# Kernel tuning notes

Hardware: AMD Instinct MI355X
Metric: run time of the kernel (lower is better)

## Reference

```python
import jax, jax.numpy as jnp
import numpy as np
import math

LMAX = 2
NUM_Z = 4
N_NODES = 20000
N_GRAPHS = 5000
N_EDGES = 320000
# irreps as (mul, l, parity)
IR_SH   = [(1, 0, 1), (1, 1, -1), (1, 2, 1)]
IR_ATTR = [(NUM_Z**2, 0, 1), (NUM_Z**2, 1, -1), (NUM_Z**2, 2, 1)]
IR_MID  = [(64, 0, 1), (24, 1, 1), (24, 1, -1), (16, 2, 1), (16, 2, -1)]
IR_OUT  = [(1, 0, -1), (6, 0, 1)]


def _cg(j1, j2, j3, m1, m2, m3):
    if m1 + m2 != m3:
        return 0.0
    f = math.factorial
    pre = math.sqrt((2 * j3 + 1) * f(j3 + j1 - j2) * f(j3 - j1 + j2) * f(j1 + j2 - j3) / f(j1 + j2 + j3 + 1))
    pre *= math.sqrt(f(j3 + m3) * f(j3 - m3) * f(j1 - m1) * f(j1 + m1) * f(j2 - m2) * f(j2 + m2))
    s = 0.0
    for k in range(max(0, j2 - j3 - m1, j1 - j3 + m2), min(j1 + j2 - j3, j1 - m1, j2 + m2) + 1):
        s += (-1) ** k / (f(k) * f(j1 + j2 - j3 - k) * f(j1 - m1 - k) * f(j2 + m2 - k) * f(j3 - j2 + m1 + k) * f(j3 - j1 - m2 + k))
    return pre * s


def _u(l):
    # complex -> real spherical harmonics change of basis, m = -l..l
    U = np.zeros((2 * l + 1, 2 * l + 1), dtype=complex)
    for m in range(-l, l + 1):
        if m > 0:
            U[m + l, -m + l] = 1 / math.sqrt(2)
            U[m + l, m + l] = (-1) ** m / math.sqrt(2)
        elif m == 0:
            U[l, l] = 1.0
        else:
            U[m + l, m + l] = 1j / math.sqrt(2)
            U[m + l, -m + l] = -1j * (-1) ** (-m) / math.sqrt(2)
    return U


def _w3j(l1, l2, l3):
    C = np.zeros((2 * l1 + 1, 2 * l2 + 1, 2 * l3 + 1))
    for m1 in range(-l1, l1 + 1):
        for m2 in range(-l2, l2 + 1):
            m3 = m1 + m2
            if -l3 <= m3 <= l3:
                C[m1 + l1, m2 + l2, m3 + l3] = _cg(l1, l2, l3, m1, m2, m3)
    T = np.einsum('am,bn,co,mno->abc', _u(l1), _u(l2), _u(l3).conj(), C.astype(complex))
    T = T.real if np.abs(T.real).max() >= np.abs(T.imag).max() else T.imag
    return (T / np.linalg.norm(T)).astype(np.float32)  # Frobenius norm 1, e3nn convention


W3J = {(a, b, c): _w3j(a, b, c) for a in range(3) for b in range(3) for c in range(3) if abs(a - b) <= c <= a + b}


def _slices(ir):
    s = [0]
    for m, l, _ in ir:
        s.append(s[-1] + m * (2 * l + 1))
    return s


def _paths(ir1, ir2, iro):
    paths = []
    fan = [0] * len(iro)
    off = 0
    for a, (m1, l1, p1) in enumerate(ir1):
        for b, (m2, l2, p2) in enumerate(ir2):
            for c, (m3, l3, p3) in enumerate(iro):
                if p1 * p2 == p3 and abs(l1 - l2) <= l3 <= l1 + l2:
                    paths.append((a, b, c, off))
                    fan[c] += m1 * m2
                    off += m1 * m2 * m3
    return paths, fan, off


def _fctp(x1, x2, w, ir1, ir2, iro):
    # FullyConnectedTensorProduct: 'uvw' weighted Clebsch-Gordan contraction per path
    s1, s2 = _slices(ir1), _slices(ir2)
    paths, fan, _ = _paths(ir1, ir2, iro)
    E = x1.shape[0]
    out = [jnp.zeros((E, m * (2 * l + 1)), x1.dtype) for m, l, _ in iro]
    for a, b, c, off in paths:
        m1, l1, _ = ir1[a]
        m2, l2, _ = ir2[b]
        m3, l3, _ = iro[c]
        W = w[off:off + m1 * m2 * m3].reshape(m1, m2, m3)
        C = jnp.asarray(W3J[(l1, l2, l3)], x1.dtype)
        xa = x1[:, s1[a]:s1[a + 1]].reshape(E, m1, 2 * l1 + 1)
        xb = x2[:, s2[b]:s2[b + 1]].reshape(E, m2, 2 * l2 + 1)
        alpha = math.sqrt(2 * l3 + 1) / math.sqrt(fan[c])
        y = jnp.einsum('eui,evj,ijk,uvw->ewk', xa, xb, C, W)
        out[c] = out[c] + (alpha * y).reshape(E, -1)
    return jnp.concatenate(out, axis=1)


def _sh(v):
    # component-normalized harmonic polynomials for l=0,1,2 (normalize=False)
    x, y, z = v[:, 0], v[:, 1], v[:, 2]
    r2 = x * x + y * y + z * z
    s3, s15, s5 = math.sqrt(3.0), math.sqrt(15.0), math.sqrt(5.0)
    sh1 = s3 * jnp.stack([y, z, x], axis=1)
    sh2 = jnp.stack([s15 * x * y, s15 * y * z, 0.5 * s5 * (3 * z * z - r2), s15 * x * z, 0.5 * s15 * (x * x - y * y)], axis=1)
    return jnp.concatenate([jnp.ones_like(x)[:, None], sh1, sh2], axis=1)  # [E, 9]


def _forward(pos, w_tp1, w_tp2, z, batch, edge_src, edge_dst):
    E = edge_src.shape[0]
    ev = pos[edge_src] - pos[edge_dst]
    sh = _sh(ev)
    zz = NUM_Z * z[edge_src] + z[edge_dst]
    zzf = jax.nn.one_hot(zz, NUM_Z ** 2, dtype=sh.dtype) * NUM_Z  # [E, 16]
    # 'uvu' TensorProduct of (16x0e) with sh: outer product per l block
    blocks = [(0, 1), (1, 4), (4, 9)]
    edge_attr = jnp.concatenate([(zzf[:, :, None] * sh[:, None, a:b]).reshape(E, -1) for a, b in blocks], axis=1)
    inv_nn = 1.0 / math.sqrt(3.0)  # num_neighbors = 3
    node = jax.ops.segment_sum(sh, edge_dst, num_segments=N_NODES) * inv_nn
    ef = _fctp(node[edge_src], edge_attr, w_tp1, IR_SH, IR_ATTR, IR_MID)
    node = jax.ops.segment_sum(ef, edge_dst, num_segments=N_NODES) * inv_nn
    ef = _fctp(node[edge_src], edge_attr, w_tp2, IR_MID, IR_ATTR, IR_OUT)
    node = jax.ops.segment_sum(ef, edge_dst, num_segments=N_NODES) * inv_nn
    return jax.ops.segment_sum(node, batch, num_segments=N_GRAPHS) * 0.5  # num_nodes = 4


def setup_inputs() -> dict:
    key = jax.random.key(0)
    k = jax.random.split(key, 7)
    _, _, n1 = _paths(IR_SH, IR_ATTR, IR_MID)
    _, _, n2 = _paths(IR_MID, IR_ATTR, IR_OUT)
    return {
        'pos': jax.random.normal(k[0], (N_NODES, 3), jnp.float32),
        'z': jax.random.randint(k[1], (N_NODES,), 0, NUM_Z, jnp.int32),
        'batch': jnp.sort(jax.random.randint(k[2], (N_NODES,), 0, N_GRAPHS, jnp.int32)),
        'edge_src': jax.random.randint(k[3], (N_EDGES,), 0, N_NODES, jnp.int32),
        'edge_dst': jax.random.randint(k[4], (N_EDGES,), 0, N_NODES, jnp.int32),
        'w_tp1': jax.random.normal(k[5], (n1,), jnp.float32),
        'w_tp2': jax.random.normal(k[6], (n2,), jnp.float32),
    }


def reference(pos, z, batch, edge_src, edge_dst, w_tp1, w_tp2):
    return _forward(pos, w_tp1, w_tp2, z, batch, edge_src, edge_dst)
```

## Files before the change

### kernel.cpp

```cpp
#include <hip/hip_runtime.h>


#define N_EDGES   320000
#define NN_NODES  20000
#define NN_GRAPHS 5000

__device__ __forceinline__ void sh_from_vec(float x, float y, float z,
                                            float* B1, float* B2) {
    const float s3   = 1.7320508075688772f;
    const float s15  = 3.8729833462074170f;
    const float s5h  = 1.1180339887498949f;
    const float s15h = 1.9364916731037085f;
    B1[0] = s3 * y; B1[1] = s3 * z; B1[2] = s3 * x;
    float r2 = x * x + y * y + z * z;
    B2[0] = s15 * x * y;
    B2[1] = s15 * y * z;
    B2[2] = s5h * (3.f * z * z - r2);
    B2[3] = s15 * x * z;
    B2[4] = s15h * (x * x - y * y);
}

__global__ __launch_bounds__(256) void k_zero(const float* __restrict__ pos,
                                              const float* __restrict__ w2,
                                              int* __restrict__ counts,
                                              float* __restrict__ out,
                                              float4* __restrict__ pos4,
                                              float* __restrict__ w2p) {
    int tid = blockIdx.x * blockDim.x + threadIdx.x;
    int stride = gridDim.x * blockDim.x;
    for (int i = tid; i < NN_NODES; i += stride) counts[i] = 0;
    for (int i = tid; i < NN_GRAPHS * 7; i += stride) out[i] = 0.f;
    for (int i = tid; i < NN_NODES; i += stride) {
        float4 p;
        p.x = pos[3 * i]; p.y = pos[3 * i + 1]; p.z = pos[3 * i + 2]; p.w = 0.f;
        pos4[i] = p;
    }
    const float cT0f =  0.02830690f;
    const float cT1f = -0.02635231f;
    const float cT2f = -0.01634300f;
    const float cT3f =  0.01265893f;
    const float cT4f =  0.02041241f;
    for (int idx = tid; idx < 16 * 64 * 64; idx += stride) {
        int jj = idx & 63;
        int u  = (idx >> 6) & 63;
        int q  = idx >> 12;
        float v = 0.f;
        if (jj < 6) {
            v = cT0f * w2[(u * 16 + q) * 6 + jj];
        } else if (jj < 9) {
            if (u < 24) v = cT1f * w2[6144 + u * 16 + q];
        } else if (jj < 27) {
            int w = (jj - 9) % 6;
            if (u < 24) v = cT2f * w2[6528 + (u * 16 + q) * 6 + w];
        } else if (jj < 57) {
            int w = (jj - 27) % 6;
            if (u < 16) v = cT3f * w2[8832 + (u * 16 + q) * 6 + w];
        } else if (jj < 62) {
            if (u < 16) v = cT4f * w2[10368 + u * 16 + q];
        }
        w2p[idx] = v;
    }
}

__global__ __launch_bounds__(256) void k_hist(const int* __restrict__ edst,
                                              int* __restrict__ counts) {
    int e = blockIdx.x * blockDim.x + threadIdx.x;
    if (e < N_EDGES) atomicAdd(&counts[edst[e]], 1);
}

__global__ __launch_bounds__(1024) void k_scan(const int* __restrict__ counts,
                                               int* __restrict__ start,
                                               int* __restrict__ cursor) {
    __shared__ int wsum[16];
    __shared__ int carry;
    __shared__ int tot;
    int tid = threadIdx.x;
    int wave = tid >> 6;
    int lane = tid & 63;
    if (tid == 0) carry = 0;
    __syncthreads();
    for (int base = 0; base < NN_NODES; base += 1024) {
        int i = base + tid;
        int v = (i < NN_NODES) ? counts[i] : 0;
        int x = v;
#pragma unroll
        for (int off = 1; off < 64; off <<= 1) {
            int y = __shfl_up(x, off, 64);
            if (lane >= off) x += y;
        }
        if (lane == 63) wsum[wave] = x;
        __syncthreads();
        if (tid < 16) {
            int w = wsum[tid];
            int xx = w;
#pragma unroll
            for (int off = 1; off < 16; off <<= 1) {
                int y = __shfl_up(xx, off, 64);
                if (tid >= off) xx += y;
            }
            wsum[tid] = xx - w;
            if (tid == 15) tot = xx;
        }
        __syncthreads();
        int excl = carry + wsum[wave] + x - v;
        if (i < NN_NODES) {
            start[i] = excl;
            cursor[i] = excl;
        }
        __syncthreads();
        if (tid == 0) carry += tot;
        __syncthreads();
    }
    if (tid == 0) start[NN_NODES] = carry;
}

__global__ __launch_bounds__(256) void k_fill(const int* __restrict__ esrc,
                                              const int* __restrict__ edst,
                                              const int* __restrict__ zarr,
                                              int* __restrict__ cursor,
                                              int* __restrict__ csr) {
    int e = blockIdx.x * blockDim.x + threadIdx.x;
    if (e >= N_EDGES) return;
    int d = edst[e];
    int s = esrc[e];
    int q = 4 * zarr[s] + zarr[d];
    int p = atomicAdd(&cursor[d], 1);
    csr[p] = s | (q << 16) | ((d & 15) << 20);
}

__global__ __launch_bounds__(256) void k_nodesh(const float4* __restrict__ pos4,
                                                const int* __restrict__ start,
                                                const int* __restrict__ csr,
                                                float* __restrict__ node_sh) {
    __shared__ float ns[16][12];
    int t = threadIdx.x;
    if (t < 192) ns[t / 12][t % 12] = 0.f;
    __syncthreads();
    int nbase = blockIdx.x * 16;
    int e0 = start[nbase], e1 = start[nbase + 16];
    for (int idx = e0 + t; idx < e1; idx += 256) {
        int pk = csr[idx];
        int s = pk & 0xFFFF;
        int r = (pk >> 20) & 15;
        float4 pd = pos4[nbase + r];
        float4 ps = pos4[s];
        float x = ps.x - pd.x;
        float y = ps.y - pd.y;
        float z = ps.z - pd.z;
        float B1[3], B2[5];
        sh_from_vec(x, y, z, B1, B2);
        float* nr = &ns[r][0];
        atomicAdd(nr + 0, 1.f);
        atomicAdd(nr + 1, B1[0]); atomicAdd(nr + 2, B1[1]); atomicAdd(nr + 3, B1[2]);
        atomicAdd(nr + 4, B2[0]); atomicAdd(nr + 5, B2[1]); atomicAdd(nr + 6, B2[2]);
        atomicAdd(nr + 7, B2[3]); atomicAdd(nr + 8, B2[4]);
    }
    __syncthreads();
    if (t < 144) {
        int r = t / 9, c = t % 9;
        const float inv_nn = 0.57735026918962576f;
        node_sh[(size_t)(nbase + r) * 12 + c] = ns[r][c] * inv_nn;
    }
}

template<int RB>
__device__ __forceinline__ void phase2_pass(const float* __restrict__ Gl,
                                            float (* __restrict__ smid)[368],
                                            const float* __restrict__ w1,
                                            int zpack, int j) {
    const int zp = zpack >> (2 * RB);
    float acc[8] = {0.f, 0.f, 0.f, 0.f, 0.f, 0.f, 0.f, 0.f};
    if (j < 64) {
        int w = j;
        for (int q = 0; q < 16; q++) {
            float wa = w1[q * 64 + w];
            float wb = w1[2048 + q * 64 + w];
            float wc = w1[5248 + q * 64 + w];
            int zdq = q & 3;
            const float* Gq = Gl + (q >> 2) * 51;
#pragma unroll
            for (int r2 = 0; r2 < 8; r2++) {
                if (((zp >> (2 * r2)) & 3) == zdq) {
                    const float* gq = Gq + (RB + r2) * 204;
                    acc[r2] += gq[0] * wa + gq[12] * wb + gq[42] * wc;
                }
            }
        }
#pragma unroll
        for (int r2 = 0; r2 < 8; r2++)
            smid[RB + r2][j] = 0.33333333333333333f * acc[r2];
    } else if (j < 136) {
        int tt = j - 64, w = tt / 3, k = tt - 3 * w;
        for (int q = 0; q < 16; q++) {
            float wa = w1[3072 + q * 24 + w];
            float wb = w1[6272 + q * 24 + w];
            int zdq = q & 3;
            const float* Gq = Gl + (q >> 2) * 51;
#pragma unroll
            for (int r2 = 0; r2 < 8; r2++) {
                if (((zp >> (2 * r2)) & 3) == zdq) {
                    const float* gq = Gq + (RB + r2) * 204;
                    acc[r2] += gq[13 + k] * wa + gq[43 + k] * wb;
                }
            }
        }
#pragma unroll
        for (int r2 = 0; r2 < 8; r2++)
            smid[RB + r2][j] = 0.70710678118654752f * acc[r2];
    } else if (j < 208) {
        int tt = j - 136, w = tt / 3, k = tt - 3 * w;
        for (int q = 0; q < 16; q++) {
            float wa = w1[1024 + q * 24 + w];
            float wb = w1[1664 + q * 24 + w];
            float wc = w1[3712 + q * 24 + w];
            float wd = w1[4608 + q * 24 + w];
            int zdq = q & 3;
            const float* Gq = Gl + (q >> 2) * 51;
#pragma unroll
            for (int r2 = 0; r2 < 8; r2++) {
                if (((zp >> (2 * r2)) & 3) == zdq) {
                    const float* gq = Gq + (RB + r2) * 204;
                    acc[r2] += gq[1 + k] * wa + gq[9 + k] * wb +
                               gq[21 + k] * wc + gq[34 + k] * wd;
                }
            }
        }
#pragma unroll
        for (int r2 = 0; r2 < 8; r2++)
            smid[RB + r2][j] = 0.5f * acc[r2];
    } else if (j < 288) {
        int tt = j - 208, w = tt / 5, k = tt - 5 * w;
        for (int q = 0; q < 16; q++) {
            float wa = w1[1408 + q * 16 + w];
            float wb = w1[3456 + q * 16 + w];
            float wc = w1[4352 + q * 16 + w];
            float wd = w1[6656 + q * 16 + w];
            int zdq = q & 3;
            const float* Gq = Gl + (q >> 2) * 51;
#pragma unroll
            for (int r2 = 0; r2 < 8; r2++) {
                if (((zp >> (2 * r2)) & 3) == zdq) {
                    const float* gq = Gq + (RB + r2) * 204;
                    acc[r2] += gq[4 + k] * wa + gq[16 + k] * wb +
                               gq[29 + k] * wc + gq[46 + k] * wd;
                }
            }
        }
#pragma unroll
        for (int r2 = 0; r2 < 8; r2++)
            smid[RB + r2][j] = 0.64549722436790280f * acc[r2];
    } else if (j < 368) {
        int tt = j - 288, w = tt / 5, k = tt - 5 * w;
        for (int q = 0; q < 16; q++) {
            float wa = w1[4096 + q * 16 + w];
            float wb = w1[4992 + q * 16 + w];
            int zdq = q & 3;
            const float* Gq = Gl + (q >> 2) * 51;
#pragma unroll
            for (int r2 = 0; r2 < 8; r2++) {
                if (((zp >> (2 * r2)) & 3) == zdq) {
                    const float* gq = Gq + (RB + r2) * 204;
                    acc[r2] += gq[24 + k] * wa + gq[37 + k] * wb;
                }
            }
        }
#pragma unroll
        for (int r2 = 0; r2 < 8; r2++)
            smid[RB + r2][j] = 0.91287092917527690f * acc[r2];
    }
}

__global__ __launch_bounds__(512, 4) void k_mid(const float4* __restrict__ pos4,
                                                const float* __restrict__ node_sh,
                                                const int* __restrict__ start,
                                                const int* __restrict__ csr,
                                                const float* __restrict__ w1,
                                                const int* __restrict__ zarr,
                                                const float* __restrict__ w2p,
                                                float* __restrict__ tab) {
    __shared__ float Gl[16 * 204];
    __shared__ float smid[16][368];
    __shared__ int szl[16];
    __shared__ int zcnt[4];
    __shared__ int zlist[4][16];
    int t = threadIdx.x;
    int nbase = blockIdx.x * 16;
    for (int i = t; i < 16 * 204; i += 512) Gl[i] = 0.f;
    if (t < 16) szl[t] = zarr[nbase + t];
    else if (t < 20) zcnt[t - 16] = 0;
    __syncthreads();

    int e0 = start[nbase], e1 = start[nbase + 16];

    const float r3  = 0.57735026918962576f;
    const float r5  = 0.44721359549995794f;
    const float r6  = 0.40824829046386302f;
    const float r10 = 0.31622776601683794f;
    const float s30 = 0.18257418583505536f;
    const float rt3 = 1.7320508075688772f;
    const float c222 = 0.58554004376911990f;
    const float q6 = 0.40824829046386302f;
    const float h6 = 0.20412414523193151f;
    const float h2 = 0.35355339059327376f;
    const float r2c = 0.70710678118654752f;

    for (int idx = e0 + t; idx < e1; idx += 512) {
        int pk = csr[idx];
        int s = pk & 0xFFFF;
        int zs = (pk >> 18) & 3;
        int r = (pk >> 20) & 15;
        float4 pd = pos4[nbase + r];
        float4 ps = pos4[s];
        float x = ps.x - pd.x;
        float y = ps.y - pd.y;
        float z = ps.z - pd.z;
        float B1[3], B2[5];
        sh_from_vec(x, y, z, B1, B2);
        const float4 nv0 = *(const float4*)(node_sh + s * 12);
        const float4 nv1 = *(const float4*)(node_sh + s * 12 + 4);
        float a0 = nv0.x;
        float A1[3] = {nv0.y, nv0.z, nv0.w};
        float A2[5] = {nv1.x, nv1.y, nv1.z, nv1.w, node_sh[s * 12 + 8]};
        float* gr = Gl + r * 204 + zs * 51;

        atomicAdd(gr + 0, a0);
        atomicAdd(gr + 1, a0 * B1[0] * r3);
        atomicAdd(gr + 2, a0 * B1[1] * r3);
        atomicAdd(gr + 3, a0 * B1[2] * r3);
        atomicAdd(gr + 4, a0 * B2[0] * r5);
        atomicAdd(gr + 5, a0 * B2[1] * r5);
        atomicAdd(gr + 6, a0 * B2[2] * r5);
        atomicAdd(gr + 7, a0 * B2[3] * r5);
        atomicAdd(gr + 8, a0 * B2[4] * r5);
        atomicAdd(gr + 9,  A1[0] * r3);
        atomicAdd(gr + 10, A1[1] * r3);
        atomicAdd(gr + 11, A1[2] * r3);
        atomicAdd(gr + 12, -r3 * (A1[0] * B1[0] + A1[1] * B1[1] + A1[2] * B1[2]));
        atomicAdd(gr + 13, -r6 * (A1[1] * B1[2] - A1[2] * B1[1]));
        atomicAdd(gr + 14, -r6 * (A1[2] * B1[0] - A1[0] * B1[2]));
        atomicAdd(gr + 15, -r6 * (A1[0] * B1[1] - A1[1] * B1[0]));
        atomicAdd(gr + 16, r10 * (A1[0] * B1[2] + A1[2] * B1[0]));
        atomicAdd(gr + 17, r10 * (A1[0] * B1[1] + A1[1] * B1[0]));
        atomicAdd(gr + 18, s30 * (2.f * A1[1] * B1[1] - A1[0] * B1[0] - A1[2] * B1[2]));
        atomicAdd(gr + 19, r10 * (A1[1] * B1[2] + A1[2] * B1[1]));
        atomicAdd(gr + 20, r10 * (A1[2] * B1[2] - A1[0] * B1[0]));
        {
            float Byy = -B2[2] * q6 - B2[4] * r2c;
            float Bzz = 2.f * B2[2] * q6;
            float Bxx = -B2[2] * q6 + B2[4] * r2c;
            float Bxy = B2[0] * r2c;
            float Byz = B2[1] * r2c;
            float Bxz = B2[3] * r2c;
            atomicAdd(gr + 21, -r5 * (Byy * A1[0] + Byz * A1[1] + Bxy * A1[2]));
            atomicAdd(gr + 22, -r5 * (Byz * A1[0] + Bzz * A1[1] + Bxz * A1[2]));
            atomicAdd(gr + 23, -r5 * (Bxy * A1[0] + Bxz * A1[1] + Bxx * A1[2]));
        }
        atomicAdd(gr + 24, -s30 * (B2[1] * A1[0] - B2[3] * A1[2] + 2.f * B2[4] * A1[1]));
        atomicAdd(gr + 25, -s30 * (-B2[0] * A1[0] - rt3 * B2[2] * A1[2] + B2[3] * A1[1] - B2[4] * A1[2]));
        atomicAdd(gr + 26, -s30 * (rt3 * B2[1] * A1[2] - rt3 * B2[3] * A1[0]));
        atomicAdd(gr + 27, -s30 * (B2[0] * A1[2] - B2[1] * A1[1] + rt3 * B2[2] * A1[0] - B2[4] * A1[0]));
        atomicAdd(gr + 28, -s30 * (-2.f * B2[0] * A1[1] + B2[1] * A1[2] + B2[3] * A1[0]));
        atomicAdd(gr + 29, A2[0] * r5);
        atomicAdd(gr + 30, A2[1] * r5);
        atomicAdd(gr + 31, A2[2] * r5);
        atomicAdd(gr + 32, A2[3] * r5);
        atomicAdd(gr + 33, A2[4] * r5);
        {
            float Ayy = -A2[2] * q6 - A2[4] * r2c;
            float Azz = 2.f * A2[2] * q6;
            float Axx = -A2[2] * q6 + A2[4] * r2c;
            float Axy = A2[0] * r2c;
            float Ayz = A2[1] * r2c;
            float Axz = A2[3] * r2c;
            atomicAdd(gr + 34, -r5 * (Ayy * B1[0] + Ayz * B1[1] + Axy * B1[2]));
            atomicAdd(gr + 35, -r5 * (Ayz * B1[0] + Azz * B1[1] + Axz * B1[2]));
            atomicAdd(gr + 36, -r5 * (Axy * B1[0] + Axz * B1[1] + Axx * B1[2]));
        }
        atomicAdd(gr + 37, s30 * (A2[1] * B1[0] - A2[3] * B1[2] + 2.f * A2[4] * B1[1]));
        atomicAdd(gr + 38, s30 * (-A2[0] * B1[0] - rt3 * A2[2] * B1[2] + A2[3] * B1[1] - A2[4] * B1[2]));
        atomicAdd(gr + 39, s30 * (rt3 * A2[1] * B1[2] - rt3 * A2[3] * B1[0]));
        atomicAdd(gr + 40, s30 * (A2[0] * B1[2] - A2[1] * B1[1] + rt3 * A2[2] * B1[0] - A2[4] * B1[0]));
        atomicAdd(gr + 41, s30 * (-2.f * A2[0] * B1[1] + A2[1] * B1[2] + A2[3] * B1[0]));
        atomicAdd(gr + 42, r5 * (A2[0] * B2[0] + A2[1] * B2[1] + A2[2] * B2[2] +
                                 A2[3] * B2[3] + A2[4] * B2[4]));
        atomicAdd(gr + 43, s30 * (-A2[0] * B2[1] + A2[1] * B2[0] +
                                  rt3 * (A2[2] * B2[3] - A2[3] * B2[2]) +
                                  A2[3] * B2[4] - A2[4] * B2[3]));
        atomicAdd(gr + 44, s30 * (-2.f * A2[0] * B2[4] + 2.f * A2[4] * B2[0] -
                                  A2[1] * B2[3] + A2[3] * B2[1]));
        atomicAdd(gr + 45, s30 * (A2[0] * B2[3] - A2[3] * B2[0] +
                                  rt3 * (A2[1] * B2[2] - A2[2] * B2[1]) +
                                  A2[1] * B2[4] - A2[4] * B2[1]));
        atomicAdd(gr + 46, -c222 * (-q6 * (A2[0] * B2[2] + A2[2] * B2[0]) +
                                    h2 * (A2[1] * B2[3] + A2[3] * B2[1])));
        atomicAdd(gr + 47, -c222 * (h6 * (A2[1] * B2[2] + A2[2] * B2[1]) -
                                    h2 * (A2[1] * B2[4] + A2[4] * B2[1]) +
                                    h2 * (A2[0] * B2[3] + A2[3] * B2[0])));
        atomicAdd(gr + 48, -c222 * (q6 * (A2[2] * B2[2] - A2[0] * B2[0] - A2[4] * B2[4]) +
                                    h6 * (A2[1] * B2[1] + A2[3] * B2[3])));
        atomicAdd(gr + 49, -c222 * (h6 * (A2[3] * B2[2] + A2[2] * B2[3]) +
                                    h2 * (A2[3] * B2[4] + A2[4] * B2[3]) +
                                    h2 * (A2[0] * B2[1] + A2[1] * B2[0])));
        atomicAdd(gr + 50, -c222 * (-q6 * (A2[4] * B2[2] + A2[2] * B2[4]) +
                                    h2 * (A2[3] * B2[3] - A2[1] * B2[1])));
    }
    __syncthreads();

    int zpack = 0;
#pragma unroll
    for (int r2 = 0; r2 < 16; r2++)
        zpack |= __builtin_amdgcn_readfirstlane(szl[r2]) << (2 * r2);

    if (t < 16) {
        int zsv = (zpack >> (2 * t)) & 3;
        int p = atomicAdd(&zcnt[zsv], 1);
        zlist[zsv][p] = t;
    }

    phase2_pass<0>(Gl, smid, w1, zpack, t);
    phase2_pass<8>(Gl, smid, w1, zpack, t);
    __syncthreads();

    {
        int wave = t >> 6;
        int lane = t & 63;
        int mbase, mstride, ulim;
        if (lane < 6)       { mbase = 0;                mstride = 1; ulim = 64; }
        else if (lane < 9)  { mbase = 64 + (lane - 6);  mstride = 3; ulim = 24; }
        else if (lane < 27) { mbase = 136 + (lane - 9) / 6;  mstride = 3; ulim = 24; }
        else if (lane < 57) { mbase = 208 + (lane - 27) / 6; mstride = 5; ulim = 16; }
        else if (lane < 62) { mbase = 288 + (lane - 57);     mstride = 5; ulim = 16; }
        else                { mbase = 0;                mstride = 0; ulim = 1; }
        int ulim1 = ulim - 1;

        int c0 = zcnt[0], c1 = zcnt[1], c2 = zcnt[2], c3 = zcnt[3];
        int np0 = (c0 + 1) >> 1, np1 = (c1 + 1) >> 1;
        int np2 = (c2 + 1) >> 1, np3 = (c3 + 1) >> 1;
        int o1 = np0, o2 = o1 + np1, o3 = o2 + np2;
        int total = o3 + np3;

        for (int item = wave; item < total; item += 8) {
            int zsv, pi, cnt;
            if (item < o1)      { zsv = 0; pi = item;      cnt = c0; }
            else if (item < o2) { zsv = 1; pi = item - o1; cnt = c1; }
            else if (item < o3) { zsv = 2; pi = item - o2; cnt = c2; }
            else                { zsv = 3; pi = item - o3; cnt = c3; }
            int r0 = zlist[zsv][2 * pi];
            int i1 = 2 * pi + 1;
            int has2 = (i1 < cnt);
            int r1 = has2 ? zlist[zsv][i1] : r0;
            const float* mr0 = &smid[r0][0];
            const float* mr1 = &smid[r1][0];
            const float* wp = w2p + (size_t)(4 * zsv) * 4096 + lane;
            float a00 = 0.f, a01 = 0.f, a02 = 0.f, a03 = 0.f;
            float a10 = 0.f, a11 = 0.f, a12 = 0.f, a13 = 0.f;
#pragma unroll 4
            for (int u = 0; u < 64; u++) {
                int um = (u < ulim) ? u : ulim1;
                float w0 = wp[u * 64];
                float w1v = wp[4096 + u * 64];
                float w2v = wp[8192 + u * 64];
                float w3v = wp[12288 + u * 64];
                float m0 = mr0[mbase + mstride * um];
                float m1 = mr1[mbase + mstride * um];
                a00 += m0 * w0;  a01 += m0 * w1v;
                a02 += m0 * w2v; a03 += m0 * w3v;
                a10 += m1 * w0;  a11 += m1 * w1v;
                a12 += m1 * w2v; a13 += m1 * w3v;
            }
            size_t b0 = ((size_t)(nbase + r0) * 4) * 64 + lane;
            tab[b0] = a00; tab[b0 + 64] = a01;
            tab[b0 + 128] = a02; tab[b0 + 192] = a03;
            if (has2) {
                size_t b1 = ((size_t)(nbase + r1) * 4) * 64 + lane;
                tab[b1] = a10; tab[b1 + 64] = a11;
                tab[b1 + 128] = a12; tab[b1 + 192] = a13;
            }
        }
    }
}

__global__ __launch_bounds__(512, 8) void k_out(const float4* __restrict__ pos4,
                                                const int* __restrict__ zarr,
                                                const int* __restrict__ batch,
                                                const int* __restrict__ start,
                                                const int* __restrict__ csr,
                                                const float* __restrict__ tab,
                                                float* __restrict__ out) {
    int wave = threadIdx.x >> 6;
    int lane = threadIdx.x & 63;
    int n = blockIdx.x * 8 + wave;
    float4 pd = pos4[n];
    int zd = zarr[n];
    int s0 = start[n], s1 = start[n + 1];

    int fsel, oidx;
    if (lane < 6)       { fsel = 0;                  oidx = lane + 1; }
    else if (lane < 9)  { fsel = 1 + (lane - 6);     oidx = 0; }
    else if (lane < 27) { fsel = 1 + (lane - 9) / 6; oidx = (lane - 9) % 6 + 1; }
    else if (lane < 57) { fsel = 4 + (lane - 27) / 6; oidx = (lane - 27) % 6 + 1; }
    else if (lane < 62) { fsel = 4 + (lane - 57);    oidx = 0; }
    else                { fsel = -1;                 oidx = 7; }
    float f0 = (fsel == 0) ? 1.f : 0.f;
    float f1 = (fsel == 1) ? 1.f : 0.f;
    float f2 = (fsel == 2) ? 1.f : 0.f;
    float f3 = (fsel == 3) ? 1.f : 0.f;
    float f4 = (fsel == 4) ? 1.f : 0.f;
    float f5 = (fsel == 5) ? 1.f : 0.f;
    float f6 = (fsel == 6) ? 1.f : 0.f;
    float f7 = (fsel == 7) ? 1.f : 0.f;
    float f8 = (fsel == 8) ? 1.f : 0.f;

    float acc = 0.f;
    int idx = s0;
    for (; idx + 1 < s1; idx += 2) {
        int pkA = __builtin_amdgcn_readfirstlane(csr[idx]);
        int pkB = __builtin_amdgcn_readfirstlane(csr[idx + 1]);
        int sA = pkA & 0xFFFF;
        int sB = pkB & 0xFFFF;
        float TA = tab[((size_t)sA * 4 + zd) * 64 + lane];
        float TB = tab[((size_t)sB * 4 + zd) * 64 + lane];
        float4 psA = pos4[sA];
        float4 psB = pos4[sB];
        float xA = psA.x - pd.x, yA = psA.y - pd.y, zA = psA.z - pd.z;
        float xB = psB.x - pd.x, yB = psB.y - pd.y, zB = psB.z - pd.z;
        float B1A[3], B2A[5], B1B[3], B2B[5];
        sh_from_vec(xA, yA, zA, B1A, B2A);
        sh_from_vec(xB, yB, zB, B1B, B2B);
        float fA = f0 + f1 * B1A[0] + f2 * B1A[1] + f3 * B1A[2]
                 + f4 * B2A[0] + f5 * B2A[1] + f6 * B2A[2]
                 + f7 * B2A[3] + f8 * B2A[4];
        float fB = f0 + f1 * B1B[0] + f2 * B1B[1] + f3 * B1B[2]
                 + f4 * B2B[0] + f5 * B2B[1] + f6 * B2B[2]
                 + f7 * B2B[3] + f8 * B2B[4];
        acc += TA * fA + TB * fB;
    }
    if (idx < s1) {
        int pk = __builtin_amdgcn_readfirstlane(csr[idx]);
        int s = pk & 0xFFFF;
        float T = tab[((size_t)s * 4 + zd) * 64 + lane];
        float4 ps = pos4[s];
        float x = ps.x - pd.x, y = ps.y - pd.y, z = ps.z - pd.z;
        float B1[3], B2[5];
        sh_from_vec(x, y, z, B1, B2);
        float factor = f0 + f1 * B1[0] + f2 * B1[1] + f3 * B1[2]
                     + f4 * B2[0] + f5 * B2[1] + f6 * B2[2]
                     + f7 * B2[3] + f8 * B2[4];
        acc += T * factor;
    }

    float ov[7];
#pragma unroll
    for (int w = 0; w < 7; w++) ov[w] = (oidx == w) ? acc : 0.f;
#pragma unroll
    for (int off = 32; off > 0; off >>= 1)
#pragma unroll
        for (int w = 0; w < 7; w++) ov[w] += __shfl_down(ov[w], off, 64);
    if (lane == 0) {
        float* og = out + batch[n] * 7;
#pragma unroll
        for (int w = 0; w < 7; w++) atomicAdd(og + w, ov[w]);
    }
}

extern "C" void kernel_launch(void* const* d_in, const int* in_sizes, int n_in,
                              void* d_out, int out_size, void* d_ws, size_t ws_size,
                              hipStream_t stream) {
    const float* pos  = (const float*)d_in[0];
    const int*   z    = (const int*)d_in[1];
    const int*   bat  = (const int*)d_in[2];
    const int*   esrc = (const int*)d_in[3];
    const int*   edst = (const int*)d_in[4];
    const float* w1   = (const float*)d_in[5];
    const float* w2   = (const float*)d_in[6];
    float* out = (float*)d_out;

    int*   wsI = (int*)d_ws;
    float* wsF = (float*)d_ws;
    int* counts  = wsI + 0;
    int* start   = wsI + 32768;
    int* cursor  = wsI + 65536;
    int* csr     = wsI + 98304;
    float4* pos4   = (float4*)(wsF + 425984);
    float* node_sh = wsF + 524288;
    float* w2p     = wsF + 786432;
    float* tab     = wsF + 1048576;

    k_zero<<<128, 256, 0, stream>>>(pos, w2, counts, out, pos4, w2p);
    k_hist<<<(N_EDGES + 255) / 256, 256, 0, stream>>>(edst, counts);
    k_scan<<<1, 1024, 0, stream>>>(counts, start, cursor);
    k_fill<<<(N_EDGES + 255) / 256, 256, 0, stream>>>(esrc, edst, z, cursor, csr);
    k_nodesh<<<NN_NODES / 16, 256, 0, stream>>>(pos4, start, csr, node_sh);
    k_mid<<<NN_NODES / 16, 512, 0, stream>>>(pos4, node_sh, start, csr, w1, z, w2p, tab);
    k_out<<<NN_NODES / 8, 512, 0, stream>>>(pos4, z, bat, start, csr, tab, out);
}
```

Baseline: 354.3 us.

## Split mid-feature contraction into separate table kernel via global buffer

Moves the per-node second-stage contraction (mid features times w2p into the 4x64 table) out of k_mid into a new k_tab kernel, with mid features written to global memory and reused in place as the table (row stride 368). This frees k_mid's large shared smid array and z-grouping logic, which could raise occupancy, and gives the contraction its own launch with one wave per node. The cost is an extra global round trip of the mid features, one more kernel launch, and the loss of the old two-node sharing of weight loads within a z-group.

```diff
diff --git a/kernel.cpp b/kernel.cpp
--- a/kernel.cpp
+++ b/kernel.cpp
@@ -165,7 +165,8 @@
 
 template<int RB>
 __device__ __forceinline__ void phase2_pass(const float* __restrict__ Gl,
-                                            float (* __restrict__ smid)[368],
+                                            float* __restrict__ mid,
+                                            int nbase,
                                             const float* __restrict__ w1,
                                             int zpack, int j) {
     const int zp = zpack >> (2 * RB);
@@ -188,7 +189,7 @@
         }
 #pragma unroll
         for (int r2 = 0; r2 < 8; r2++)
-            smid[RB + r2][j] = 0.33333333333333333f * acc[r2];
+            mid[(size_t)(nbase + RB + r2) * 368 + j] = 0.33333333333333333f * acc[r2];
     } else if (j < 136) {
         int tt = j - 64, w = tt / 3, k = tt - 3 * w;
         for (int q = 0; q < 16; q++) {
@@ -206,7 +207,7 @@
         }
 #pragma unroll
         for (int r2 = 0; r2 < 8; r2++)
-            smid[RB + r2][j] = 0.70710678118654752f * acc[r2];
+            mid[(size_t)(nbase + RB + r2) * 368 + j] = 0.70710678118654752f * acc[r2];
     } else if (j < 208) {
         int tt = j - 136, w = tt / 3, k = tt - 3 * w;
         for (int q = 0; q < 16; q++) {
@@ -227,7 +228,7 @@
         }
 #pragma unroll
         for (int r2 = 0; r2 < 8; r2++)
-            smid[RB + r2][j] = 0.5f * acc[r2];
+            mid[(size_t)(nbase + RB + r2) * 368 + j] = 0.5f * acc[r2];
     } else if (j < 288) {
         int tt = j - 208, w = tt / 5, k = tt - 5 * w;
         for (int q = 0; q < 16; q++) {
@@ -248,7 +249,7 @@
         }
 #pragma unroll
         for (int r2 = 0; r2 < 8; r2++)
-            smid[RB + r2][j] = 0.64549722436790280f * acc[r2];
+            mid[(size_t)(nbase + RB + r2) * 368 + j] = 0.64549722436790280f * acc[r2];
     } else if (j < 368) {
         int tt = j - 288, w = tt / 5, k = tt - 5 * w;
         for (int q = 0; q < 16; q++) {
@@ -266,7 +267,7 @@
         }
 #pragma unroll
         for (int r2 = 0; r2 < 8; r2++)
-            smid[RB + r2][j] = 0.91287092917527690f * acc[r2];
+            mid[(size_t)(nbase + RB + r2) * 368 + j] = 0.91287092917527690f * acc[r2];
     }
 }
 
@@ -276,18 +277,13 @@
                                                 const int* __restrict__ csr,
                                                 const float* __restrict__ w1,
                                                 const int* __restrict__ zarr,
-                                                const float* __restrict__ w2p,
-                                                float* __restrict__ tab) {
+                                                float* __restrict__ mid) {
     __shared__ float Gl[16 * 204];
-    __shared__ float smid[16][368];
     __shared__ int szl[16];
-    __shared__ int zcnt[4];
-    __shared__ int zlist[4][16];
     int t = threadIdx.x;
     int nbase = blockIdx.x * 16;
     for (int i = t; i < 16 * 204; i += 512) Gl[i] = 0.f;
     if (t < 16) szl[t] = zarr[nbase + t];
-    else if (t < 20) zcnt[t - 16] = 0;
     __syncthreads();
 
     int e0 = start[nbase], e1 = start[nbase + 16];
@@ -411,73 +407,51 @@
     for (int r2 = 0; r2 < 16; r2++)
         zpack |= __builtin_amdgcn_readfirstlane(szl[r2]) << (2 * r2);
 
-    if (t < 16) {
-        int zsv = (zpack >> (2 * t)) & 3;
-        int p = atomicAdd(&zcnt[zsv], 1);
-        zlist[zsv][p] = t;
-    }
-
-    phase2_pass<0>(Gl, smid, w1, zpack, t);
-    phase2_pass<8>(Gl, smid, w1, zpack, t);
+    phase2_pass<0>(Gl, mid, nbase, w1, zpack, t);
+    phase2_pass<8>(Gl, mid, nbase, w1, zpack, t);
+}
+
+__global__ __launch_bounds__(256, 8) void k_tab(const int* __restrict__ zarr,
+                                                const float* __restrict__ w2p,
+                                                float* __restrict__ mid) {
+    __shared__ float srow[4][368];
+    int t = threadIdx.x;
+    int nbase = blockIdx.x * 4;
+    for (int i = t; i < 4 * 368; i += 256) {
+        int r = i / 368, c = i - r * 368;
+        srow[r][c] = mid[(size_t)(nbase + r) * 368 + c];
+    }
     __syncthreads();
 
-    {
-        int wave = t >> 6;
-        int lane = t & 63;
-        int mbase, mstride, ulim;
-        if (lane < 6)       { mbase = 0;                mstride = 1; ulim = 64; }
-        else if (lane < 9)  { mbase = 64 + (lane - 6);  mstride = 3; ulim = 24; }
-        else if (lane < 27) { mbase = 136 + (lane - 9) / 6;  mstride = 3; ulim = 24; }
-        else if (lane < 57) { mbase = 208 + (lane - 27) / 6; mstride = 5; ulim = 16; }
-        else if (lane < 62) { mbase = 288 + (lane - 57);     mstride = 5; ulim = 16; }
-        else                { mbase = 0;                mstride = 0; ulim = 1; }
-        int ulim1 = ulim - 1;
-
-        int c0 = zcnt[0], c1 = zcnt[1], c2 = zcnt[2], c3 = zcnt[3];
-        int np0 = (c0 + 1) >> 1, np1 = (c1 + 1) >> 1;
-        int np2 = (c2 + 1) >> 1, np3 = (c3 + 1) >> 1;
-        int o1 = np0, o2 = o1 + np1, o3 = o2 + np2;
-        int total = o3 + np3;
-
-        for (int item = wave; item < total; item += 8) {
-            int zsv, pi, cnt;
-            if (item < o1)      { zsv = 0; pi = item;      cnt = c0; }
-            else if (item < o2) { zsv = 1; pi = item - o1; cnt = c1; }
-            else if (item < o3) { zsv = 2; pi = item - o2; cnt = c2; }
-            else                { zsv = 3; pi = item - o3; cnt = c3; }
-            int r0 = zlist[zsv][2 * pi];
-            int i1 = 2 * pi + 1;
-            int has2 = (i1 < cnt);
-            int r1 = has2 ? zlist[zsv][i1] : r0;
-            const float* mr0 = &smid[r0][0];
-            const float* mr1 = &smid[r1][0];
-            const float* wp = w2p + (size_t)(4 * zsv) * 4096 + lane;
-            float a00 = 0.f, a01 = 0.f, a02 = 0.f, a03 = 0.f;
-            float a10 = 0.f, a11 = 0.f, a12 = 0.f, a13 = 0.f;
+    int wave = t >> 6;
+    int lane = t & 63;
+    int n = nbase + wave;
+    int zs = zarr[n];
+    int mbase, mstride, ulim;
+    if (lane < 6)       { mbase = 0;                mstride = 1; ulim = 64; }
+    else if (lane < 9)  { mbase = 64 + (lane - 6);  mstride = 3; ulim = 24; }
+    else if (lane < 27) { mbase = 136 + (lane - 9) / 6;  mstride = 3; ulim = 24; }
+    else if (lane < 57) { mbase = 208 + (lane - 27) / 6; mstride = 5; ulim = 16; }
+    else if (lane < 62) { mbase = 288 + (lane - 57);     mstride = 5; ulim = 16; }
+    else                { mbase = 0;                mstride = 0; ulim = 1; }
+    int ulim1 = ulim - 1;
+    const float* mr = &srow[wave][0];
+    const float* wp = w2p + (size_t)(4 * zs) * 4096 + lane;
+    float a0 = 0.f, a1 = 0.f, a2 = 0.f, a3 = 0.f;
 #pragma unroll 4
-            for (int u = 0; u < 64; u++) {
-                int um = (u < ulim) ? u : ulim1;
-                float w0 = wp[u * 64];
-                float w1v = wp[4096 + u * 64];
-                float w2v = wp[8192 + u * 64];
-                float w3v = wp[12288 + u * 64];
-                float m0 = mr0[mbase + mstride * um];
-                float m1 = mr1[mbase + mstride * um];
-                a00 += m0 * w0;  a01 += m0 * w1v;
-                a02 += m0 * w2v; a03 += m0 * w3v;
-                a10 += m1 * w0;  a11 += m1 * w1v;
-                a12 += m1 * w2v; a13 += m1 * w3v;
-            }
-            size_t b0 = ((size_t)(nbase + r0) * 4) * 64 + lane;
-            tab[b0] = a00; tab[b0 + 64] = a01;
-            tab[b0 + 128] = a02; tab[b0 + 192] = a03;
-            if (has2) {
-                size_t b1 = ((size_t)(nbase + r1) * 4) * 64 + lane;
-                tab[b1] = a10; tab[b1 + 64] = a11;
-                tab[b1 + 128] = a12; tab[b1 + 192] = a13;
-            }
-        }
-    }
+    for (int u = 0; u < 64; u++) {
+        int um = (u < ulim) ? u : ulim1;
+        float m = mr[mbase + mstride * um];
+        a0 += m * wp[u * 64];
+        a1 += m * wp[4096 + u * 64];
+        a2 += m * wp[8192 + u * 64];
+        a3 += m * wp[12288 + u * 64];
+    }
+    float* trow = mid + (size_t)n * 368;
+    trow[lane]       = a0;
+    trow[64 + lane]  = a1;
+    trow[128 + lane] = a2;
+    trow[192 + lane] = a3;
 }
 
 __global__ __launch_bounds__(512, 8) void k_out(const float4* __restrict__ pos4,
@@ -511,6 +485,7 @@
     float f7 = (fsel == 7) ? 1.f : 0.f;
     float f8 = (fsel == 8) ? 1.f : 0.f;
 
+    int zoff = zd * 64 + lane;
     float acc = 0.f;
     int idx = s0;
     for (; idx + 1 < s1; idx += 2) {
@@ -518,8 +493,8 @@
         int pkB = __builtin_amdgcn_readfirstlane(csr[idx + 1]);
         int sA = pkA & 0xFFFF;
         int sB = pkB & 0xFFFF;
-        float TA = tab[((size_t)sA * 4 + zd) * 64 + lane];
-        float TB = tab[((size_t)sB * 4 + zd) * 64 + lane];
+        float TA = tab[(size_t)sA * 368 + zoff];
+        float TB = tab[(size_t)sB * 368 + zoff];
         float4 psA = pos4[sA];
         float4 psB = pos4[sB];
         float xA = psA.x - pd.x, yA = psA.y - pd.y, zA = psA.z - pd.z;
@@ -538,7 +513,7 @@
     if (idx < s1) {
         int pk = __builtin_amdgcn_readfirstlane(csr[idx]);
         int s = pk & 0xFFFF;
-        float T = tab[((size_t)s * 4 + zd) * 64 + lane];
+        float T = tab[(size_t)s * 368 + zoff];
         float4 ps = pos4[s];
         float x = ps.x - pd.x, y = ps.y - pd.y, z = ps.z - pd.z;
         float B1[3], B2[5];
@@ -584,13 +559,14 @@
     float4* pos4   = (float4*)(wsF + 425984);
     float* node_sh = wsF + 524288;
     float* w2p     = wsF + 786432;
-    float* tab     = wsF + 1048576;
+    float* mid     = wsF + 1048576;
 
     k_zero<<<128, 256, 0, stream>>>(pos, w2, counts, out, pos4, w2p);
     k_hist<<<(N_EDGES + 255) / 256, 256, 0, stream>>>(edst, counts);
     k_scan<<<1, 1024, 0, stream>>>(counts, start, cursor);
     k_fill<<<(N_EDGES + 255) / 256, 256, 0, stream>>>(esrc, edst, z, cursor, csr);
     k_nodesh<<<NN_NODES / 16, 256, 0, stream>>>(pos4, start, csr, node_sh);
-    k_mid<<<NN_NODES / 16, 512, 0, stream>>>(pos4, node_sh, start, csr, w1, z, w2p, tab);
-    k_out<<<NN_NODES / 8, 512, 0, stream>>>(pos4, z, bat, start, csr, tab, out);
-}
+    k_mid<<<NN_NODES / 16, 512, 0, stream>>>(pos4, node_sh, start, csr, w1, z, mid);
+    k_tab<<<NN_NODES / 4, 256, 0, stream>>>(z, w2p, mid);
+    k_out<<<NN_NODES / 8, 512, 0, stream>>>(pos4, z, bat, start, csr, mid, out);
+}
```

Result: slower. 379.2 us (+7.0%).
